# Kernel optimization log

Measured on AMD Instinct MI355X. Metric: run time of the kernel, lower is better.

The kernel has to match this reference:

```python
import jax, jax.numpy as jnp
import numpy as np

B = 256           # puzzles per batch
C = 128           # hidden_channels
L = 8             # num_layers
H, D = 4, 32      # heads, out per head (H*D == C, concat=True)
N_CELLS = 81
EPS_LN = 1e-5
NEG_SLOPE = 0.2   # PyG GATv2Conv default


def _sudoku_edges():
    # replicates GNNModel._create_sudoku_edges: row0=src, row1=dst, 1620 edges
    edges = []
    for r in range(9):
        for c in range(9):
            src = r * 9 + c
            nb = set()
            for k in range(9):
                if k != c:
                    nb.add(r * 9 + k)
                if k != r:
                    nb.add(k * 9 + c)
            br, bc = r // 3, c // 3
            for i in range(br * 3, br * 3 + 3):
                for j in range(bc * 3, bc * 3 + 3):
                    if i != r or j != c:
                        nb.add(i * 9 + j)
            for d in sorted(nb):
                edges.append((src, d))
    return np.array(edges, dtype=np.int32).T  # [2, 1620]


def setup_inputs() -> dict:
    key = jax.random.key(0)
    ks = jax.random.split(key, 8)
    base = _sudoku_edges()                                   # [2, 1620]
    shift = np.arange(B, dtype=np.int32) * N_CELLS
    ei = (base[:, None, :] + shift[None, :, None]).reshape(2, -1)  # [2, B*1620]
    s = 1.0 / np.sqrt(C)
    return {
        "x": jax.random.randint(ks[0], (B, 9, 9), 0, 10, dtype=jnp.int32),
        "edge_index": jnp.asarray(ei),
        "embed_w": jax.random.normal(ks[1], (10, C), jnp.float32) * 0.1,
        "Wl": jax.random.normal(ks[2], (L, C, C), jnp.float32) * s,
        "bl": jnp.zeros((L, C), jnp.float32),
        "Wr": jax.random.normal(ks[3], (L, C, C), jnp.float32) * s,
        "br": jnp.zeros((L, C), jnp.float32),
        "att": jax.random.normal(ks[4], (L, H, D), jnp.float32) * 0.1,
        "conv_b": jnp.zeros((L, C), jnp.float32),
        "ln_w": jnp.ones((L, C), jnp.float32),
        "ln_b": jnp.zeros((L, C), jnp.float32),
        "cls_w": jax.random.normal(ks[5], (C, 9), jnp.float32) * s,
        "cls_b": jnp.zeros((9,), jnp.float32),
    }


def _segment_softmax(logits, seg, n):
    # numerically stable per-destination-node softmax (PyG softmax semantics)
    m = jax.ops.segment_max(logits, seg, num_segments=n)
    e = jnp.exp(logits - m[seg])
    s = jax.ops.segment_sum(e, seg, num_segments=n)
    return e / (s[seg] + 1e-16)


def reference(x, edge_index, embed_w, Wl, bl, Wr, br, att, conv_b,
              ln_w, ln_b, cls_w, cls_b):
    N = B * N_CELLS
    h = embed_w[x.reshape(-1)]                               # [N, C]
    src, dst = edge_index[0], edge_index[1]
    for l in range(L):  # fixed small layer count
        h_in = h
        xl = (h @ Wl[l] + bl[l]).reshape(N, H, D)            # lin_l(x) -> values/src
        xr = (h @ Wr[l] + br[l]).reshape(N, H, D)            # lin_r(x) -> dst
        e = jax.nn.leaky_relu(xl[src] + xr[dst], NEG_SLOPE)  # [E, H, D]
        logits = jnp.einsum('ehd,hd->eh', e, att[l])         # [E, H]
        alpha = _segment_softmax(logits, dst, N)             # [E, H]
        out = jax.ops.segment_sum(xl[src] * alpha[..., None], dst,
                                  num_segments=N)            # [N, H, D]
        out = out.reshape(N, C) + conv_b[l]
        # PyG LayerNorm(mode='graph') with batch=None: global mean/std
        g = out - out.mean()
        g = g / (g.std() + EPS_LN)
        h = jax.nn.relu(g * ln_w[l] + ln_b[l]) + h_in        # dropout off (eval)
    logits = h @ cls_w + cls_b                               # [N, 9]
    return logits.reshape(B, 9, 9, 9)
```

## Files before the change

### kernel.cpp

```cpp
#include <hip/hip_runtime.h>
#include <string.h>

#define NPZ 81
#define NNODES 20736
#define CH 128
#define NHEAD 4
#define NB 20
#define NLAY 8
#define TPB 768

typedef __attribute__((ext_vector_type(4))) float f32x4;
typedef __attribute__((ext_vector_type(8))) __bf16 bf16x8;
typedef __attribute__((ext_vector_type(8))) unsigned short u16x8;

#define SW(n, hh, c4) ((c4) ^ (((n) & 7) ^ ((hh) << 1)))

__device__ __forceinline__ unsigned short f2bf(float f) {
  unsigned int u = __float_as_uint(f);
  u = (u + 0x7fffu + ((u >> 16) & 1u)) >> 16;
  return (unsigned short)u;
}

struct alignas(16) Slot { float s1, s2; unsigned int flag; unsigned int pad; };

__launch_bounds__(TPB, 3)
__global__ void k_fused(const int* __restrict__ x, const float* __restrict__ ew,
                        const float* __restrict__ Wl, const float* __restrict__ bl,
                        const float* __restrict__ Wr, const float* __restrict__ br,
                        const float* __restrict__ att, const float* __restrict__ convb,
                        const float* __restrict__ lnw, const float* __restrict__ lnb,
                        const float* __restrict__ clsw, const float* __restrict__ clsb,
                        u16x8* __restrict__ wpk, Slot* __restrict__ slots,
                        float* __restrict__ logits) {
  __shared__ float h_f[NPZ * 128];
  __shared__ unsigned short h_s[NPZ * 136];
  __shared__ float xl_s[NPZ * 128];
  __shared__ float xr_s[NPZ * 128];
  __shared__ int nb_s[NPZ * NB];
  __shared__ float att6_s[CH], att4_s[CH], cvb_s[CH], bias_s[256], lnw_s[CH], lnb_s[CH];
  __shared__ float al_s[NPZ * 4];
  __shared__ float red_s[26];

  const int tid = threadIdx.x;
  const int pz = blockIdx.x;
  const int n0 = pz * NPZ;

  if (tid < NPZ) {
    const int r = tid / 9, cq = tid % 9;
    int c2 = tid * NB;
    for (int k = 0; k < 9; ++k) if (k != cq) nb_s[c2++] = r * 9 + k;
    for (int k = 0; k < 9; ++k) if (k != r) nb_s[c2++] = k * 9 + cq;
    const int br0 = (r / 3) * 3, bc0 = (cq / 3) * 3;
    for (int i = br0; i < br0 + 3; ++i)
      for (int jj = bc0; jj < bc0 + 3; ++jj)
        if (i != r && jj != cq) nb_s[c2++] = i * 9 + jj;
  }

  for (int m = tid; m < NPZ * 32; m += TPB) {
    const int j = m >> 5, c4 = m & 31;
    const int xv = x[n0 + j];
    const f32x4 v = ((const f32x4*)ew)[xv * 32 + c4];
    *(f32x4*)&h_f[j * 128 + c4 * 4] = v;
    const unsigned int lo = (unsigned int)f2bf(v[0]) | ((unsigned int)f2bf(v[1]) << 16);
    const unsigned int hi = (unsigned int)f2bf(v[2]) | ((unsigned int)f2bf(v[3]) << 16);
    *(uint2*)&h_s[j * 136 + c4 * 4] = make_uint2(lo, hi);
  }

  if (tid < 128) {
    const int t = pz * 128 + tid;
    const int lane = t & 63;
    const int kb = (t >> 6) & 3;
    const int nt = (t >> 8) & 15;
    const int l = t >> 12;
    const int cc = nt * 16 + (lane & 15);
    const int k0 = kb * 32 + (lane >> 4) * 8;
    const float* W = (cc < CH) ? (Wl + (size_t)l * CH * CH + cc)
                               : (Wr + (size_t)l * CH * CH + (cc - CH));
    u16x8 v;
#pragma unroll
    for (int e = 0; e < 8; ++e) v[e] = f2bf(W[(size_t)(k0 + e) * CH]);
    unsigned long long w0, w1;
    memcpy(&w0, &v, 8);
    memcpy(&w1, ((const char*)&v) + 8, 8);
    unsigned long long* dst = (unsigned long long*)&wpk[t];
    __hip_atomic_store(&dst[0], w0, __ATOMIC_RELAXED, __HIP_MEMORY_SCOPE_AGENT);
    __hip_atomic_store(&dst[1], w1, __ATOMIC_RELAXED, __HIP_MEMORY_SCOPE_AGENT);
  }

  __syncthreads();
  if (tid == 0)
    __hip_atomic_store(&slots[8 * 256 + pz].flag, 1u, __ATOMIC_RELAXED, __HIP_MEMORY_SCOPE_AGENT);
  if (tid < 64) {
    bool done = false;
    while (!done) {
      bool ok = true;
#pragma unroll
      for (int q = 0; q < 4; ++q)
        ok &= (__hip_atomic_load(&slots[8 * 256 + tid + q * 64].flag, __ATOMIC_RELAXED,
                                 __HIP_MEMORY_SCOPE_AGENT) == 1u);
      done = __all(ok);
      if (!done) __builtin_amdgcn_s_sleep(1);
    }
  }
  __syncthreads();

  const int wv = tid >> 6, lane = tid & 63;
  const int l15 = lane & 15, l4 = lane >> 4;
  const int p = tid >> 1, half = tid & 1;
  const int j = p >> 2, hh = p & 3;
#define CQ(q) (hh * 32 + ((((q) << 1) | half) << 2))

#pragma unroll 1
  for (int l = 0; l < NLAY; ++l) {
    if (tid < 256) bias_s[tid] = (tid < CH) ? bl[l * CH + tid] : br[l * CH + tid - CH];
    else if (tid < 384) att6_s[tid - 256] = att[l * CH + (tid - 256)] * 0.6f;
    else if (tid < 512) att4_s[tid - 384] = att[l * CH + (tid - 384)] * 0.4f;
    else if (tid < 640) cvb_s[tid - 512] = convb[l * CH + (tid - 512)];
    else lnw_s[tid - 640] = lnw[l * CH + (tid - 640)];
    if (tid < 128) lnb_s[tid] = lnb[l * CH + tid];
    __syncthreads();

#pragma unroll 1
    for (int pass = 0; pass < 2; ++pass) {
      if (pass == 1 && wv >= 4) break;
      const int nt = (pass == 0) ? wv : 12 + wv;
      bf16x8 bfr[4];
#pragma unroll
      for (int kb = 0; kb < 4; ++kb)
        bfr[kb] = ((const bf16x8*)wpk)[(((size_t)l * 16 + nt) * 4 + kb) * 64 + lane];
#pragma unroll
      for (int mt = 0; mt < 6; ++mt) {
        int arow = mt * 16 + l15; arow = arow > 80 ? 80 : arow;
        bf16x8 afr[4];
#pragma unroll
        for (int kb = 0; kb < 4; ++kb)
          afr[kb] = *(const bf16x8*)&h_s[arow * 136 + kb * 32 + l4 * 8];
        f32x4 acc = {0.f, 0.f, 0.f, 0.f};
#pragma unroll
        for (int kb = 0; kb < 4; ++kb)
          acc = __builtin_amdgcn_mfma_f32_16x16x32_bf16(afr[kb], bfr[kb], acc, 0, 0, 0);
        const int cc = nt * 16 + l15;
        const float bia = bias_s[cc];
        float* dst = (cc < CH) ? xl_s : xr_s;
        const int c127 = cc & 127;
        const int dh = c127 >> 5;
        const int c4 = (c127 >> 2) & 7, el = c127 & 3;
#pragma unroll
        for (int i = 0; i < 4; ++i) {
          const int row = mt * 16 + l4 * 4 + i;
          if (row < NPZ)
            dst[row * 128 + dh * 32 + SW(row, dh, c4) * 4 + el] = acc[i] + bia;
        }
      }
    }
    __syncthreads();

    f32x4 xr4[4], ar[4], o[4];
    float arj = 0.f;
    if (tid < NPZ * NHEAD * 2) {
      float alp = 0.f, arp = 0.f;
#pragma unroll
      for (int q = 0; q < 4; ++q) {
        const int c4 = (q << 1) | half;
        xr4[q] = *(const f32x4*)&xr_s[j * 128 + hh * 32 + SW(j, hh, c4) * 4];
        ar[q] = *(const f32x4*)&att4_s[CQ(q)];
        const f32x4 xv = *(const f32x4*)&xl_s[j * 128 + hh * 32 + SW(j, hh, c4) * 4];
        const f32x4 a6 = *(const f32x4*)&att6_s[CQ(q)];
#pragma unroll
        for (int e = 0; e < 4; ++e) {
          alp = fmaf(a6[e], xv[e], alp);
          arp = fmaf(a6[e], xr4[q][e], arp);
        }
      }
      alp += __shfl_xor(alp, 1, 64);
      arj = arp + __shfl_xor(arp, 1, 64);
      if (half == 0) al_s[j * 4 + hh] = alp;
    }
    __syncthreads();

    float psum = 0.f, psumsq = 0.f;
    if (tid < NPZ * NHEAD * 2) {
      float m = -3.0e38f, ssum = 0.f;
      f32x4 oacc[4] = {};
      for (int k = 0; k < NB; k += 2) {
        const int2 nbp = *(const int2*)&nb_s[j * NB + k];
        f32x4 v1[4], v2[4];
        float pa = 0.f, pb = 0.f;
#pragma unroll
        for (int q = 0; q < 4; ++q) {
          const int c4 = (q << 1) | half;
          v1[q] = *(const f32x4*)&xl_s[nbp.x * 128 + hh * 32 + SW(nbp.x, hh, c4) * 4];
          v2[q] = *(const f32x4*)&xl_s[nbp.y * 128 + hh * 32 + SW(nbp.y, hh, c4) * 4];
#pragma unroll
          for (int e = 0; e < 4; ++e) {
            pa = fmaf(ar[q][e], fabsf(v1[q][e] + xr4[q][e]), pa);
            pb = fmaf(ar[q][e], fabsf(v2[q][e] + xr4[q][e]), pb);
          }
        }
        const float lgA = al_s[nbp.x * 4 + hh] + arj + (pa + __shfl_xor(pa, 1, 64));
        const float lgB = al_s[nbp.y * 4 + hh] + arj + (pb + __shfl_xor(pb, 1, 64));
        const float nm = fmaxf(m, fmaxf(lgA, lgB));
        const float sc = __expf(m - nm);
        const float eA = __expf(lgA - nm);
        const float eB = __expf(lgB - nm);
        ssum = fmaf(ssum, sc, eA + eB);
#pragma unroll
        for (int q = 0; q < 4; ++q) {
          f32x4 t = oacc[q] * sc;
          t = v1[q] * eA + t;
          t = v2[q] * eB + t;
          oacc[q] = t;
        }
        m = nm;
      }
      const float rs = 1.f / ssum;
#pragma unroll
      for (int q = 0; q < 4; ++q) {
        o[q] = oacc[q] * rs + *(const f32x4*)&cvb_s[CQ(q)];
        psum += (o[q][0] + o[q][1]) + (o[q][2] + o[q][3]);
        psumsq += (o[q][0] * o[q][0] + o[q][1] * o[q][1]) +
                  (o[q][2] * o[q][2] + o[q][3] * o[q][3]);
      }
    }

#pragma unroll
    for (int mm = 1; mm < 64; mm <<= 1) {
      psum += __shfl_xor(psum, mm, 64);
      psumsq += __shfl_xor(psumsq, mm, 64);
    }
    if ((tid & 63) == 0) { red_s[wv * 2] = psum; red_s[wv * 2 + 1] = psumsq; }
    __syncthreads();

    if (tid >= 704) {
      const int pl = tid - 704;
      if (tid == 704) {
        float a = 0.f, b = 0.f;
#pragma unroll
        for (int i = 0; i < 12; ++i) { a += red_s[i * 2]; b += red_s[i * 2 + 1]; }
        Slot* sl = &slots[l * 256 + pz];
        const float2 f2 = make_float2(a, b);
        unsigned long long uv;
        memcpy(&uv, &f2, 8);
        __hip_atomic_store((unsigned long long*)&sl->s1, uv, __ATOMIC_RELAXED, __HIP_MEMORY_SCOPE_AGENT);
        asm volatile("s_waitcnt vmcnt(0)" ::: "memory");
        __hip_atomic_store(&sl->flag, 1u, __ATOMIC_RELAXED, __HIP_MEMORY_SCOPE_AGENT);
      }
      bool done = false;
      while (!done) {
        bool ok = true;
#pragma unroll
        for (int q = 0; q < 4; ++q)
          ok &= (__hip_atomic_load(&slots[l * 256 + pl + q * 64].flag, __ATOMIC_RELAXED,
                                   __HIP_MEMORY_SCOPE_AGENT) == 1u);
        done = __all(ok);
        if (!done) __builtin_amdgcn_s_sleep(1);
      }
      float s1 = 0.f, s2 = 0.f;
#pragma unroll
      for (int q = 0; q < 4; ++q) {
        const unsigned long long uv = __hip_atomic_load(
            (unsigned long long*)&slots[l * 256 + pl + q * 64].s1, __ATOMIC_RELAXED,
            __HIP_MEMORY_SCOPE_AGENT);
        float2 f2;
        memcpy(&f2, &uv, 8);
        s1 += f2.x; s2 += f2.y;
      }
#pragma unroll
      for (int mm = 1; mm < 64; mm <<= 1) {
        s1 += __shfl_xor(s1, mm, 64);
        s2 += __shfl_xor(s2, mm, 64);
      }
      if (tid == 704) {
        const float M = (float)NNODES * CH;
        const float mean = s1 / M;
        const float var = fmaxf(s2 / M - mean * mean, 0.f);
        red_s[24] = mean;
        red_s[25] = 1.f / (sqrtf(var) + 1e-5f);
      }
    }
    __syncthreads();
    const float mean = red_s[24], inv = red_s[25];

    if (tid < NPZ * NHEAD * 2) {
#pragma unroll
      for (int q = 0; q < 4; ++q) {
        const int cb = CQ(q);
        f32x4 hv = *(f32x4*)&h_f[j * 128 + cb];
#pragma unroll
        for (int e = 0; e < 4; ++e) {
          const float g = (o[q][e] - mean) * inv;
          hv[e] += fmaxf(g * lnw_s[cb + e] + lnb_s[cb + e], 0.f);
        }
        *(f32x4*)&h_f[j * 128 + cb] = hv;
        const unsigned int lo = (unsigned int)f2bf(hv[0]) | ((unsigned int)f2bf(hv[1]) << 16);
        const unsigned int hi = (unsigned int)f2bf(hv[2]) | ((unsigned int)f2bf(hv[3]) << 16);
        *(uint2*)&h_s[j * 136 + cb] = make_uint2(lo, hi);
      }
    }
    __syncthreads();
  }

  for (int idx = tid; idx < CH * 9; idx += TPB) {
    const int k = idx / 9, c = idx - k * 9;
    xr_s[k * 12 + c] = clsw[idx];
  }
  __syncthreads();
  for (int t2 = tid; t2 < NPZ * 9; t2 += TPB) {
    const int j2 = t2 / 9, c = t2 - j2 * 9;
    const int kc0 = tid & 31;
    float acc = clsb[c];
#pragma unroll 8
    for (int kc = 0; kc < 32; ++kc) {
      const int cc4 = (kc0 + kc) & 31;
      const f32x4 hv = *(const f32x4*)&h_f[j2 * 128 + cc4 * 4];
      acc += hv[0] * xr_s[(cc4 * 4 + 0) * 12 + c] + hv[1] * xr_s[(cc4 * 4 + 1) * 12 + c] +
             hv[2] * xr_s[(cc4 * 4 + 2) * 12 + c] + hv[3] * xr_s[(cc4 * 4 + 3) * 12 + c];
    }
    logits[(size_t)(n0 + j2) * 9 + c] = acc;
  }
}

extern "C" void kernel_launch(void* const* d_in, const int* in_sizes, int n_in,
                              void* d_out, int out_size, void* d_ws, size_t ws_size,
                              hipStream_t stream) {
  const int* x = (const int*)d_in[0];
  const float* ew = (const float*)d_in[2];
  const float* Wl = (const float*)d_in[3];
  const float* bl = (const float*)d_in[4];
  const float* Wr = (const float*)d_in[5];
  const float* br = (const float*)d_in[6];
  const float* att = (const float*)d_in[7];
  const float* cvb = (const float*)d_in[8];
  const float* lnw = (const float*)d_in[9];
  const float* lnb = (const float*)d_in[10];
  const float* clsw = (const float*)d_in[11];
  const float* clsb = (const float*)d_in[12];

  char* ws = (char*)d_ws;
  u16x8* wpk = (u16x8*)ws;
  Slot* slots = (Slot*)(ws + 524288);
  float* logits = (float*)d_out;

  (void)hipMemsetAsync(ws + 524288, 0, 9 * 256 * 16, stream);

  void* args[] = {(void*)&x, (void*)&ew, (void*)&Wl, (void*)&bl, (void*)&Wr, (void*)&br,
                  (void*)&att, (void*)&cvb, (void*)&lnw, (void*)&lnb, (void*)&clsw,
                  (void*)&clsb, (void*)&wpk, (void*)&slots, (void*)&logits};
  (void)hipLaunchCooperativeKernel((void*)k_fused, dim3(256), dim3(TPB), args, 0, stream);
}
```

Measured before the change: 170.6 us.

## Balance MFMA tiles across waves and prefetch next-layer params into registers

The 96 output tiles (16 column tiles × 6 row tiles) are now split evenly across the 12 waves, 8 tiles each, instead of a second pass run by only 4 waves. Each wave now loads two B-fragment sets, which adds register pressure. Per-layer parameters are prefetched into a register one layer ahead, so their global load latency overlaps compute rather than stalling before the barrier. The neighbor aggregation loop is also fully unrolled, which may grow code size and register use.

```diff
diff --git a/kernel.cpp b/kernel.cpp
--- a/kernel.cpp
+++ b/kernel.cpp
@@ -22,6 +22,17 @@
 }
 
 struct alignas(16) Slot { float s1, s2; unsigned int flag; unsigned int pad; };
+
+__device__ __forceinline__ float ldparam(int l, int s, const float* bl, const float* br,
+                                         const float* att, const float* convb,
+                                         const float* lnw, const float* lnb) {
+  if (s < 128) return bl[l * CH + s];
+  if (s < 256) return br[l * CH + s - 128];
+  if (s < 384) return att[l * CH + s - 256];
+  if (s < 512) return convb[l * CH + s - 384];
+  if (s < 640) return lnw[l * CH + s - 512];
+  return lnb[l * CH + s - 640];
+}
 
 __launch_bounds__(TPB, 3)
 __global__ void k_fused(const int* __restrict__ x, const float* __restrict__ ew,
@@ -45,6 +56,8 @@
   const int pz = blockIdx.x;
   const int n0 = pz * NPZ;
 
+  float pv = ldparam(0, tid, bl, br, att, convb, lnw, lnb);
+
   if (tid < NPZ) {
     const int r = tid / 9, cq = tid % 9;
     int c2 = tid * NB;
@@ -112,45 +125,51 @@
 
 #pragma unroll 1
   for (int l = 0; l < NLAY; ++l) {
-    if (tid < 256) bias_s[tid] = (tid < CH) ? bl[l * CH + tid] : br[l * CH + tid - CH];
-    else if (tid < 384) att6_s[tid - 256] = att[l * CH + (tid - 256)] * 0.6f;
-    else if (tid < 512) att4_s[tid - 384] = att[l * CH + (tid - 384)] * 0.4f;
-    else if (tid < 640) cvb_s[tid - 512] = convb[l * CH + (tid - 512)];
-    else lnw_s[tid - 640] = lnw[l * CH + (tid - 640)];
-    if (tid < 128) lnb_s[tid] = lnb[l * CH + tid];
-    __syncthreads();
-
-#pragma unroll 1
-    for (int pass = 0; pass < 2; ++pass) {
-      if (pass == 1 && wv >= 4) break;
-      const int nt = (pass == 0) ? wv : 12 + wv;
-      bf16x8 bfr[4];
+    const int u0 = wv * 8;
+    const int nt0 = u0 / 6;
+    const int mt0 = u0 - nt0 * 6;
+    const int split = 6 - mt0;
+    bf16x8 b0[4], b1[4];
+#pragma unroll
+    for (int kb = 0; kb < 4; ++kb) {
+      b0[kb] = ((const bf16x8*)wpk)[(((size_t)l * 16 + nt0) * 4 + kb) * 64 + lane];
+      b1[kb] = ((const bf16x8*)wpk)[(((size_t)l * 16 + nt0 + 1) * 4 + kb) * 64 + lane];
+    }
+
+    if (tid < 256) bias_s[tid] = pv;
+    else if (tid < 384) { att6_s[tid - 256] = pv * 0.6f; att4_s[tid - 256] = pv * 0.4f; }
+    else if (tid < 512) cvb_s[tid - 384] = pv;
+    else if (tid < 640) lnw_s[tid - 512] = pv;
+    else lnb_s[tid - 640] = pv;
+    __syncthreads();
+
+    pv = ldparam((l < 7) ? l + 1 : 7, tid, bl, br, att, convb, lnw, lnb);
+
+#pragma unroll
+    for (int k = 0; k < 8; ++k) {
+      const int nt = (k < split) ? nt0 : nt0 + 1;
+      const int mt = (k < split) ? mt0 + k : mt0 + k - 6;
+      int arow = mt * 16 + l15; arow = arow > 80 ? 80 : arow;
+      bf16x8 afr[4];
 #pragma unroll
       for (int kb = 0; kb < 4; ++kb)
-        bfr[kb] = ((const bf16x8*)wpk)[(((size_t)l * 16 + nt) * 4 + kb) * 64 + lane];
-#pragma unroll
-      for (int mt = 0; mt < 6; ++mt) {
-        int arow = mt * 16 + l15; arow = arow > 80 ? 80 : arow;
-        bf16x8 afr[4];
-#pragma unroll
-        for (int kb = 0; kb < 4; ++kb)
-          afr[kb] = *(const bf16x8*)&h_s[arow * 136 + kb * 32 + l4 * 8];
-        f32x4 acc = {0.f, 0.f, 0.f, 0.f};
-#pragma unroll
-        for (int kb = 0; kb < 4; ++kb)
-          acc = __builtin_amdgcn_mfma_f32_16x16x32_bf16(afr[kb], bfr[kb], acc, 0, 0, 0);
-        const int cc = nt * 16 + l15;
-        const float bia = bias_s[cc];
-        float* dst = (cc < CH) ? xl_s : xr_s;
-        const int c127 = cc & 127;
-        const int dh = c127 >> 5;
-        const int c4 = (c127 >> 2) & 7, el = c127 & 3;
-#pragma unroll
-        for (int i = 0; i < 4; ++i) {
-          const int row = mt * 16 + l4 * 4 + i;
-          if (row < NPZ)
-            dst[row * 128 + dh * 32 + SW(row, dh, c4) * 4 + el] = acc[i] + bia;
-        }
+        afr[kb] = *(const bf16x8*)&h_s[arow * 136 + kb * 32 + l4 * 8];
+      f32x4 acc = {0.f, 0.f, 0.f, 0.f};
+#pragma unroll
+      for (int kb = 0; kb < 4; ++kb)
+        acc = __builtin_amdgcn_mfma_f32_16x16x32_bf16(afr[kb], (k < split) ? b0[kb] : b1[kb],
+                                                      acc, 0, 0, 0);
+      const int cc = nt * 16 + l15;
+      const float bia = bias_s[cc];
+      float* dst = (cc < CH) ? xl_s : xr_s;
+      const int c127 = cc & 127;
+      const int dh = c127 >> 5;
+      const int c4 = (c127 >> 2) & 7, el = c127 & 3;
+#pragma unroll
+      for (int i = 0; i < 4; ++i) {
+        const int row = mt * 16 + l4 * 4 + i;
+        if (row < NPZ)
+          dst[row * 128 + dh * 32 + SW(row, dh, c4) * 4 + el] = acc[i] + bia;
       }
     }
     __syncthreads();
@@ -182,6 +201,7 @@
     if (tid < NPZ * NHEAD * 2) {
       float m = -3.0e38f, ssum = 0.f;
       f32x4 oacc[4] = {};
+#pragma unroll
       for (int k = 0; k < NB; k += 2) {
         const int2 nbp = *(const int2*)&nb_s[j * NB + k];
         f32x4 v1[4], v2[4];
```

Result: slower. 196.7 us (+15.3%).
